# Kernel optimization log

Measured on AMD Instinct MI355X. Metric: run time of the kernel, lower is better.

The kernel has to match this reference:

```python
import jax, jax.numpy as jnp
import numpy as np

HID, KQ, V = 1024, 64, 64
B, S = 8, 2048
NEG_INF = -1000000000.0


def setup_inputs() -> dict:
    key = jax.random.key(0)
    ks = jax.random.split(key, 10)
    return {
        "k_hidden_inputs": jax.random.normal(ks[0], (B, S, HID), jnp.float32),
        "q_hidden_inputs": jax.random.normal(ks[1], (B, S, HID), jnp.float32),
        "v_hidden_inputs": jax.random.normal(ks[2], (B, S, HID), jnp.float32),
        "mask": jax.random.randint(ks[3], (B, S, S), 0, 2, jnp.int32),
        "Wq": jax.random.normal(ks[4], (HID, KQ), jnp.float32) * 0.02,
        "bq": jnp.zeros((KQ,), jnp.float32),
        "Wk": jax.random.normal(ks[5], (HID, KQ), jnp.float32) * 0.02,
        "bk": jnp.zeros((KQ,), jnp.float32),
        "Wv": jax.random.normal(ks[6], (HID, V), jnp.float32) * 0.02,
        "bv": jnp.zeros((V,), jnp.float32),
    }


def reference(k_hidden_inputs, q_hidden_inputs, v_hidden_inputs, mask,
              Wq, bq, Wk, bk, Wv, bv):
    keys = jnp.einsum('bsh,hd->bsd', k_hidden_inputs, Wk) + bk
    queries = jnp.einsum('bsh,hd->bsd', q_hidden_inputs, Wq) + bq
    values = jnp.einsum('bsh,hd->bsd', v_hidden_inputs, Wv) + bv
    # scaled dot-product scores: [B, S_q, S_k]
    scores = jnp.einsum('bqd,bkd->bqk', queries, keys) / jnp.sqrt(jnp.float32(KQ))
    scores = jnp.where(mask == 0, jnp.float32(NEG_INF), scores)
    attn = jax.nn.softmax(scores, axis=-1)
    return jnp.einsum('bqk,bkv->bqv', attn, values)
```

## Files before the change

### kernel.cpp

```cpp
#include <hip/hip_runtime.h>

#define HIDDEN 1024
#define NB 8
#define SEQ 2048
#define DH 64

typedef long long i64;
typedef unsigned short u16;
typedef __attribute__((ext_vector_type(8))) _Float16 half8;
typedef __attribute__((ext_vector_type(4))) float f32x4;

#define MFMA16F __builtin_amdgcn_mfma_f32_16x16x32_f16

__device__ __forceinline__ u16 f2h(float x) {
    _Float16 h = (_Float16)x;
    return __builtin_bit_cast(u16, h);
}
__device__ __forceinline__ void gl_lds16(const void* g, void* l) {
    __builtin_amdgcn_global_load_lds(
        (const __attribute__((address_space(1))) unsigned int*)g,
        (__attribute__((address_space(3))) unsigned int*)l, 16, 0, 0);
}

__global__ __launch_bounds__(256) void wimg_prep(
    const float* __restrict__ Wq, const float* __restrict__ Wk, const float* __restrict__ Wv,
    u16* __restrict__ Wimg)
{
    const int t = blockIdx.x * 256 + threadIdx.x;
    const int te = t >> 13;
    const int rem = t & 8191;
    const int n = rem >> 7;
    const int bb = rem & 127;
    const int kq = bb >> 5, bq = bb & 31;
    const float* W = te == 0 ? Wq : te == 1 ? Wk : Wv;
    const i64 base = ((i64)(te * 4 + kq) * 64 + n) * 256 + ((bq ^ (n & 7)) << 3);
    #pragma unroll
    for (int j = 0; j < 8; ++j) {
        const int k = kq * 256 + bq * 8 + j;
        Wimg[base + j] = f2h(W[(i64)k * DH + n]);
    }
}

__global__ __launch_bounds__(256) void proj_mfma7(
    const float* __restrict__ qh, const float* __restrict__ kh, const float* __restrict__ vh,
    const u16* __restrict__ Wimg,
    const float* __restrict__ bq, const float* __restrict__ bk, const float* __restrict__ bv,
    u16* __restrict__ Qb, u16* __restrict__ Kb, u16* __restrict__ Vt)
{
    const int te = blockIdx.y;
    const float* A    = te == 0 ? qh : te == 1 ? kh : vh;
    const float* bias = te == 0 ? bq : te == 1 ? bk : bv;
    const int row0 = blockIdx.x << 6;
    const int t = threadIdx.x;
    const int w = t >> 6, lane = t & 63;
    const int lr = lane & 15, lg = lane >> 4;

    __shared__ __attribute__((aligned(16))) u16 Wl[16384];

    const u16* Wte = Wimg + (i64)te * 4 * 16384;
    const float* arow = A + (i64)(row0 + w * 16 + lr) * HIDDEN + (lg << 3);

    f32x4 acc[4] = {};

    float4 buf0[2], buf1[2];
    buf0[0] = *(const float4*)(arow);
    buf0[1] = *(const float4*)(arow + 4);
    buf1[0] = *(const float4*)(arow + 32);
    buf1[1] = *(const float4*)(arow + 36);

#define CVT8(bf, a8) { \
        const float xs_[8] = {bf[0].x, bf[0].y, bf[0].z, bf[0].w, \
                              bf[1].x, bf[1].y, bf[1].z, bf[1].w}; \
        _Pragma("unroll") \
        for (int j_ = 0; j_ < 8; ++j_) a8[j_] = (_Float16)xs_[j_]; }

    #pragma unroll 1
    for (int kq = 0; kq < 4; ++kq) {
        if (kq) __syncthreads();
        {
            const u16* src = Wte + kq * 16384 + (w << 12) + (lane << 3);
            #pragma unroll
            for (int i = 0; i < 8; ++i)
                gl_lds16(src + i * 512, &Wl[(w << 12) + i * 512]);
        }
        asm volatile("s_waitcnt vmcnt(0)" ::: "memory");
        __syncthreads();

        #pragma unroll
        for (int s = 0; s < 8; ++s) {
            const int ks = kq * 8 + s;
            half8 a;
            if ((s & 1) == 0) {
                CVT8(buf0, a)
                const int kn = ((ks + 2) & 31) << 5;
                buf0[0] = *(const float4*)(arow + kn);
                buf0[1] = *(const float4*)(arow + kn + 4);
            } else {
                CVT8(buf1, a)
                const int kn = ((ks + 2) & 31) << 5;
                buf1[0] = *(const float4*)(arow + kn);
                buf1[1] = *(const float4*)(arow + kn + 4);
            }
            const int s4 = s << 2;
            #pragma unroll
            for (int nt = 0; nt < 4; ++nt) {
                const int n = nt * 16 + lr;
                const half8 b = *(const half8*)&Wl[n * 256 + (((s4 + lg) ^ (n & 7)) << 3)];
                acc[nt] = MFMA16F(a, b, acc[nt], 0, 0, 0);
            }
        }
    }
#undef CVT8

    #pragma unroll
    for (int nt = 0; nt < 4; ++nt) {
        const int col = nt * 16 + lr;
        const float bb = bias[col];
        #pragma unroll
        for (int r = 0; r < 4; ++r) {
            const i64 grow = row0 + w * 16 + (lg << 2) + r;
            const u16 v = f2h(acc[nt][r] + bb);
            if (te == 0)      Qb[grow * DH + col] = v;
            else if (te == 1) Kb[grow * DH + col] = v;
            else {
                const i64 bb2 = grow >> 11, key = grow & 2047;
                Vt[(bb2 * DH + col) * SEQ + key] = v;
            }
        }
    }
}

__global__ __launch_bounds__(64) void attn_mfma(
    const u16* __restrict__ Qb, const u16* __restrict__ Kb, const u16* __restrict__ Vt,
    const int* __restrict__ mask, float* __restrict__ out)
{
    __shared__ __attribute__((aligned(16))) u16 Kl[2][64 * 64];
    __shared__ __attribute__((aligned(16))) u16 Vl[2][64 * 64];
    __shared__ __attribute__((aligned(16))) u16 Pl[16][72];

    const int lane = threadIdx.x;
    const int lr = lane & 15, lg = lane >> 4;
    const int b  = blockIdx.x >> 7;
    const int q0 = (blockIdx.x & 127) << 4;

    const i64 qrow = (i64)b * SEQ + q0 + lr;
    const half8 qf0 = *(const half8*)(Qb + qrow * DH + lg * 8);
    const half8 qf1 = *(const half8*)(Qb + qrow * DH + 32 + lg * 8);

    const int srow = lane >> 3;
    const int scb  = lane & 7;

    f32x4 oacc[4] = {};
    float rs0 = 0.f, rs1 = 0.f, rs2 = 0.f, rs3 = 0.f;

    {
        const i64 kbase = (i64)b * SEQ;
        #pragma unroll
        for (int i = 0; i < 8; ++i) {
            int row = i * 8 + srow, cb = scb ^ (row & 7);
            gl_lds16(Kb + (kbase + row) * DH + cb * 8, &Kl[0][i * 512]);
        }
        #pragma unroll
        for (int i = 0; i < 8; ++i) {
            int row = i * 8 + srow, cb = scb ^ (row & 7);
            gl_lds16(Vt + ((i64)b * DH + row) * SEQ + cb * 8, &Vl[0][i * 512]);
        }
    }

    #pragma unroll 1
    for (int t = 0; t < 32; ++t) {
        const int kt = t * 64;
        const int buf = t & 1;

        int mv[16];
        #pragma unroll
        for (int tt = 0; tt < 4; ++tt)
            #pragma unroll
            for (int r = 0; r < 4; ++r)
                mv[tt * 4 + r] =
                    mask[((i64)b * SEQ + q0 + lg * 4 + r) * SEQ + kt + tt * 16 + lr];

        if (t < 31) {
            const int kn = kt + 64;
            const i64 kbase = (i64)b * SEQ + kn;
            #pragma unroll
            for (int i = 0; i < 8; ++i) {
                int row = i * 8 + srow, cb = scb ^ (row & 7);
                gl_lds16(Kb + (kbase + row) * DH + cb * 8, &Kl[buf ^ 1][i * 512]);
            }
            #pragma unroll
            for (int i = 0; i < 8; ++i) {
                int row = i * 8 + srow, cb = scb ^ (row & 7);
                gl_lds16(Vt + ((i64)b * DH + row) * SEQ + kn + cb * 8, &Vl[buf ^ 1][i * 512]);
            }
            asm volatile("s_waitcnt vmcnt(32)" ::: "memory");
        } else {
            asm volatile("s_waitcnt vmcnt(16)" ::: "memory");
        }

        f32x4 sacc[4] = {};
        #pragma unroll
        for (int tt = 0; tt < 4; ++tt) {
            int row = tt * 16 + lr, x = row & 7;
            half8 k0 = *(const half8*)&Kl[buf][row * 64 + ((lg) ^ x) * 8];
            half8 k1 = *(const half8*)&Kl[buf][row * 64 + ((lg + 4) ^ x) * 8];
            sacc[tt] = MFMA16F(qf0, k0, sacc[tt], 0, 0, 0);
            sacc[tt] = MFMA16F(qf1, k1, sacc[tt], 0, 0, 0);
        }

        #pragma unroll
        for (int tt = 0; tt < 4; ++tt) {
            #pragma unroll
            for (int r = 0; r < 4; ++r) {
                float p = (mv[tt * 4 + r] != 0) ? __expf(sacc[tt][r] * 0.125f) : 0.0f;
                if      (r == 0) rs0 += p;
                else if (r == 1) rs1 += p;
                else if (r == 2) rs2 += p;
                else             rs3 += p;
                Pl[lg * 4 + r][tt * 16 + lr] = f2h(p);
            }
        }

        const half8 p0 = *(const half8*)&Pl[lr][lg * 8];
        const half8 p1 = *(const half8*)&Pl[lr][32 + lg * 8];
        #pragma unroll
        for (int vt = 0; vt < 4; ++vt) {
            int row = vt * 16 + lr, x = row & 7;
            half8 v0 = *(const half8*)&Vl[buf][row * 64 + ((lg) ^ x) * 8];
            half8 v1 = *(const half8*)&Vl[buf][row * 64 + ((lg + 4) ^ x) * 8];
            oacc[vt] = MFMA16F(p0, v0, oacc[vt], 0, 0, 0);
            oacc[vt] = MFMA16F(p1, v1, oacc[vt], 0, 0, 0);
        }
    }

    float rs[4] = {rs0, rs1, rs2, rs3};
    #pragma unroll
    for (int r = 0; r < 4; ++r) {
        float v = rs[r];
        v += __shfl_xor(v, 1, 64);
        v += __shfl_xor(v, 2, 64);
        v += __shfl_xor(v, 4, 64);
        v += __shfl_xor(v, 8, 64);
        rs[r] = 1.0f / v;
    }
    #pragma unroll
    for (int vt = 0; vt < 4; ++vt)
        #pragma unroll
        for (int r = 0; r < 4; ++r)
            out[((i64)b * SEQ + q0 + lg * 4 + r) * DH + vt * 16 + lr] = oacc[vt][r] * rs[r];
}

extern "C" void kernel_launch(void* const* d_in, const int* in_sizes, int n_in,
                              void* d_out, int out_size, void* d_ws, size_t ws_size,
                              hipStream_t stream) {
    const float* kh   = (const float*)d_in[0];
    const float* qh   = (const float*)d_in[1];
    const float* vh   = (const float*)d_in[2];
    const int*   mask = (const int*)  d_in[3];
    const float* Wq   = (const float*)d_in[4];
    const float* bq   = (const float*)d_in[5];
    const float* Wk   = (const float*)d_in[6];
    const float* bk   = (const float*)d_in[7];
    const float* Wv   = (const float*)d_in[8];
    const float* bv   = (const float*)d_in[9];
    float* out = (float*)d_out;

    u16* Wimg = (u16*)d_ws;
    u16* Qb   = Wimg + 3 * 4 * 16384;
    u16* Kb   = Qb + (i64)NB * SEQ * DH;
    u16* Vt   = Kb + (i64)NB * SEQ * DH;

    wimg_prep<<<96, 256, 0, stream>>>(Wq, Wk, Wv, Wimg);
    proj_mfma7<<<dim3(256, 3), 256, 0, stream>>>(qh, kh, vh, Wimg,
                                                 bq, bk, bv, Qb, Kb, Vt);
    attn_mfma<<<1024, 64, 0, stream>>>(Qb, Kb, Vt, mask, out);
}
```

Baseline: 120.9 us.

## Restructure projection GEMM with double-buffered LDS staging of activations and weights

The projection kernel now stages both the fp32 activation tile and the fp16 weight tile into LDS with async global-to-LDS loads, double-buffered over 8 K-chunks of 128. Previously only the weights went through LDS and activations were register-prefetched from global. Blocks are halved to 32 rows, each wave owning a 16x32 output sub-tile, which doubles the grid to 1536 blocks. The weight image layout is reorganised into 128-wide K chunks to match. This aims to overlap memory loads with MFMA work and raise occupancy, at the cost of more LDS use per block and reading each weight chunk twice as often.

```diff
diff --git a/kernel.cpp b/kernel.cpp
--- a/kernel.cpp
+++ b/kernel.cpp
@@ -22,26 +22,27 @@
         (__attribute__((address_space(3))) unsigned int*)l, 16, 0, 0);
 }
 
-__global__ __launch_bounds__(256) void wimg_prep(
+__global__ __launch_bounds__(256) void wimg_prep8(
     const float* __restrict__ Wq, const float* __restrict__ Wk, const float* __restrict__ Wv,
     u16* __restrict__ Wimg)
 {
     const int t = blockIdx.x * 256 + threadIdx.x;
     const int te = t >> 13;
     const int rem = t & 8191;
-    const int n = rem >> 7;
-    const int bb = rem & 127;
-    const int kq = bb >> 5, bq = bb & 31;
+    const int p = rem >> 10;
+    const int rem2 = rem & 1023;
+    const int n = rem2 >> 4;
+    const int pos = rem2 & 15;
     const float* W = te == 0 ? Wq : te == 1 ? Wk : Wv;
-    const i64 base = ((i64)(te * 4 + kq) * 64 + n) * 256 + ((bq ^ (n & 7)) << 3);
-    #pragma unroll
-    for (int j = 0; j < 8; ++j) {
-        const int k = kq * 256 + bq * 8 + j;
-        Wimg[base + j] = f2h(W[(i64)k * DH + n]);
-    }
-}
-
-__global__ __launch_bounds__(256) void proj_mfma7(
+    const int g = pos ^ (n & 7);
+    const int k0 = p * 128 + g * 8;
+    u16* dst = Wimg + (i64)t * 8;
+    #pragma unroll
+    for (int j = 0; j < 8; ++j)
+        dst[j] = f2h(W[(i64)(k0 + j) * DH + n]);
+}
+
+__global__ __launch_bounds__(256) void proj_mfma8(
     const float* __restrict__ qh, const float* __restrict__ kh, const float* __restrict__ vh,
     const u16* __restrict__ Wimg,
     const float* __restrict__ bq, const float* __restrict__ bk, const float* __restrict__ bv,
@@ -50,75 +51,82 @@
     const int te = blockIdx.y;
     const float* A    = te == 0 ? qh : te == 1 ? kh : vh;
     const float* bias = te == 0 ? bq : te == 1 ? bk : bv;
-    const int row0 = blockIdx.x << 6;
+    const int row0 = blockIdx.x << 5;
     const int t = threadIdx.x;
     const int w = t >> 6, lane = t & 63;
     const int lr = lane & 15, lg = lane >> 4;
-
-    __shared__ __attribute__((aligned(16))) u16 Wl[16384];
-
-    const u16* Wte = Wimg + (i64)te * 4 * 16384;
-    const float* arow = A + (i64)(row0 + w * 16 + lr) * HIDDEN + (lg << 3);
-
-    f32x4 acc[4] = {};
-
-    float4 buf0[2], buf1[2];
-    buf0[0] = *(const float4*)(arow);
-    buf0[1] = *(const float4*)(arow + 4);
-    buf1[0] = *(const float4*)(arow + 32);
-    buf1[1] = *(const float4*)(arow + 36);
-
-#define CVT8(bf, a8) { \
-        const float xs_[8] = {bf[0].x, bf[0].y, bf[0].z, bf[0].w, \
-                              bf[1].x, bf[1].y, bf[1].z, bf[1].w}; \
+    const int wr = (w & 1) << 4;
+    const int wc = (w >> 1) << 5;
+
+    __shared__ __attribute__((aligned(16))) float AL[2][32 * 128];
+    __shared__ __attribute__((aligned(16))) u16  WL[2][64 * 128];
+
+    const u16* Wte = Wimg + (i64)te * 8 * 8192;
+
+    const float* asrc[4]; int adst[4];
+    #pragma unroll
+    for (int i = 0; i < 4; ++i) {
+        const int r0 = 8 * w + 2 * i;
+        const int rl = r0 + (lane >> 5);
+        asrc[i] = A + (i64)(row0 + rl) * HIDDEN + (((lane & 31) ^ (rl & 7)) << 2);
+        adst[i] = r0 * 128;
+    }
+    const u16* wsrc[4]; int wdst[4];
+    #pragma unroll
+    for (int i = 0; i < 4; ++i) {
+        const int n0 = 16 * w + 4 * i;
+        wsrc[i] = Wte + n0 * 128 + (lane << 3);
+        wdst[i] = n0 * 128;
+    }
+
+    f32x4 acc[2] = {};
+
+#define STAGE8(bufi, p) { \
         _Pragma("unroll") \
-        for (int j_ = 0; j_ < 8; ++j_) a8[j_] = (_Float16)xs_[j_]; }
-
+        for (int i_ = 0; i_ < 4; ++i_) \
+            gl_lds16(asrc[i_] + (p) * 128, &AL[bufi][adst[i_]]); \
+        _Pragma("unroll") \
+        for (int i_ = 0; i_ < 4; ++i_) \
+            gl_lds16(wsrc[i_] + (p) * 8192, &WL[bufi][wdst[i_]]); }
+
+    STAGE8(0, 0)
+
+    int buf = 0;
     #pragma unroll 1
-    for (int kq = 0; kq < 4; ++kq) {
-        if (kq) __syncthreads();
-        {
-            const u16* src = Wte + kq * 16384 + (w << 12) + (lane << 3);
-            #pragma unroll
-            for (int i = 0; i < 8; ++i)
-                gl_lds16(src + i * 512, &Wl[(w << 12) + i * 512]);
-        }
+    for (int p = 0; p < 8; ++p) {
         asm volatile("s_waitcnt vmcnt(0)" ::: "memory");
         __syncthreads();
-
-        #pragma unroll
-        for (int s = 0; s < 8; ++s) {
-            const int ks = kq * 8 + s;
+        if (p < 7) STAGE8(buf ^ 1, p + 1)
+        const int x = lr & 7;
+        #pragma unroll
+        for (int ks = 0; ks < 4; ++ks) {
+            const int b0 = ks * 8 + lg * 2;
+            const float4 fa = *(const float4*)&AL[buf][(wr + lr) * 128 + ((b0 ^ x) << 2)];
+            const float4 fb = *(const float4*)&AL[buf][(wr + lr) * 128 + (((b0 + 1) ^ x) << 2)];
             half8 a;
-            if ((s & 1) == 0) {
-                CVT8(buf0, a)
-                const int kn = ((ks + 2) & 31) << 5;
-                buf0[0] = *(const float4*)(arow + kn);
-                buf0[1] = *(const float4*)(arow + kn + 4);
-            } else {
-                CVT8(buf1, a)
-                const int kn = ((ks + 2) & 31) << 5;
-                buf1[0] = *(const float4*)(arow + kn);
-                buf1[1] = *(const float4*)(arow + kn + 4);
-            }
-            const int s4 = s << 2;
-            #pragma unroll
-            for (int nt = 0; nt < 4; ++nt) {
-                const int n = nt * 16 + lr;
-                const half8 b = *(const half8*)&Wl[n * 256 + (((s4 + lg) ^ (n & 7)) << 3)];
-                acc[nt] = MFMA16F(a, b, acc[nt], 0, 0, 0);
-            }
-        }
-    }
-#undef CVT8
-
-    #pragma unroll
-    for (int nt = 0; nt < 4; ++nt) {
-        const int col = nt * 16 + lr;
+            a[0] = (_Float16)fa.x; a[1] = (_Float16)fa.y;
+            a[2] = (_Float16)fa.z; a[3] = (_Float16)fa.w;
+            a[4] = (_Float16)fb.x; a[5] = (_Float16)fb.y;
+            a[6] = (_Float16)fb.z; a[7] = (_Float16)fb.w;
+            #pragma unroll
+            for (int nt = 0; nt < 2; ++nt) {
+                const int n = wc + nt * 16 + lr;
+                const int pos = (ks * 4 + lg) ^ x;
+                const half8 bfr = *(const half8*)&WL[buf][n * 128 + (pos << 3)];
+                acc[nt] = MFMA16F(a, bfr, acc[nt], 0, 0, 0);
+            }
+        }
+        buf ^= 1;
+    }
+#undef STAGE8
+
+    #pragma unroll
+    for (int nt = 0; nt < 2; ++nt) {
+        const int col = wc + nt * 16 + lr;
         const float bb = bias[col];
         #pragma unroll
         for (int r = 0; r < 4; ++r) {
-            const i64 grow = row0 + w * 16 + (lg << 2) + r;
+            const i64 grow = row0 + wr + (lg << 2) + r;
             const u16 v = f2h(acc[nt][r] + bb);
             if (te == 0)      Qb[grow * DH + col] = v;
             else if (te == 1) Kb[grow * DH + col] = v;
@@ -266,12 +274,12 @@
     float* out = (float*)d_out;
 
     u16* Wimg = (u16*)d_ws;
-    u16* Qb   = Wimg + 3 * 4 * 16384;
+    u16* Qb   = Wimg + 3 * 8 * 8192;
     u16* Kb   = Qb + (i64)NB * SEQ * DH;
     u16* Vt   = Kb + (i64)NB * SEQ * DH;
 
-    wimg_prep<<<96, 256, 0, stream>>>(Wq, Wk, Wv, Wimg);
-    proj_mfma7<<<dim3(256, 3), 256, 0, stream>>>(qh, kh, vh, Wimg,
+    wimg_prep8<<<96, 256, 0, stream>>>(Wq, Wk, Wv, Wimg);
+    proj_mfma8<<<dim3(512, 3), 256, 0, stream>>>(qh, kh, vh, Wimg,
                                                  bq, bk, bv, Qb, Kb, Vt);
     attn_mfma<<<1024, 64, 0, stream>>>(Qb, Kb, Vt, mask, out);
 }
```

Result: faster. 115.0 us (-4.9%).

## Double-buffer weight chunks in LDS with smaller projection blocks

Applied to the files above, without the earlier changes.

The projection kernel now works on 32 rows per block with 128 threads, and it walks K in 16 chunks of 64. Weight chunks are staged into two alternating LDS buffers, and the next chunk's activations are prefetched while the current chunk is computed. The weight image is re-laid out into 64-wide K chunks with an XOR swizzle to match. The goal is to overlap global weight staging with MFMA work, shrink LDS use from 32KB to 16KB per block, and raise the number of blocks in flight. In exchange there are more barriers per row tile, and weight traffic per row doubles. The code also has no explicit vmcnt wait before the barrier, so it depends on in-order completion of the vector memory loads.

```diff
diff --git a/kernel.cpp b/kernel.cpp
--- a/kernel.cpp
+++ b/kernel.cpp
@@ -22,26 +22,27 @@
         (__attribute__((address_space(3))) unsigned int*)l, 16, 0, 0);
 }
 
-__global__ __launch_bounds__(256) void wimg_prep(
+__global__ __launch_bounds__(256) void wimg_prep16(
     const float* __restrict__ Wq, const float* __restrict__ Wk, const float* __restrict__ Wv,
     u16* __restrict__ Wimg)
 {
     const int t = blockIdx.x * 256 + threadIdx.x;
     const int te = t >> 13;
     const int rem = t & 8191;
-    const int n = rem >> 7;
-    const int bb = rem & 127;
-    const int kq = bb >> 5, bq = bb & 31;
+    const int p = rem >> 9;
+    const int rem2 = rem & 511;
+    const int n = rem2 >> 3;
+    const int pos = rem2 & 7;
     const float* W = te == 0 ? Wq : te == 1 ? Wk : Wv;
-    const i64 base = ((i64)(te * 4 + kq) * 64 + n) * 256 + ((bq ^ (n & 7)) << 3);
-    #pragma unroll
-    for (int j = 0; j < 8; ++j) {
-        const int k = kq * 256 + bq * 8 + j;
-        Wimg[base + j] = f2h(W[(i64)k * DH + n]);
-    }
-}
-
-__global__ __launch_bounds__(256) void proj_mfma7(
+    const int g = pos ^ (n & 7);
+    const int k0 = p * 64 + g * 8;
+    u16* dst = Wimg + (i64)t * 8;
+    #pragma unroll
+    for (int j = 0; j < 8; ++j)
+        dst[j] = f2h(W[(i64)(k0 + j) * DH + n]);
+}
+
+__global__ __launch_bounds__(128) void proj_mfma9(
     const float* __restrict__ qh, const float* __restrict__ kh, const float* __restrict__ vh,
     const u16* __restrict__ Wimg,
     const float* __restrict__ bq, const float* __restrict__ bk, const float* __restrict__ bv,
@@ -50,67 +51,81 @@
     const int te = blockIdx.y;
     const float* A    = te == 0 ? qh : te == 1 ? kh : vh;
     const float* bias = te == 0 ? bq : te == 1 ? bk : bv;
-    const int row0 = blockIdx.x << 6;
+    const int row0 = blockIdx.x << 5;
     const int t = threadIdx.x;
     const int w = t >> 6, lane = t & 63;
     const int lr = lane & 15, lg = lane >> 4;
 
-    __shared__ __attribute__((aligned(16))) u16 Wl[16384];
-
-    const u16* Wte = Wimg + (i64)te * 4 * 16384;
+    __shared__ __attribute__((aligned(16))) u16 WL[2][4096];
+
+    const u16* Wte = Wimg + (i64)te * 16 * 4096;
     const float* arow = A + (i64)(row0 + w * 16 + lr) * HIDDEN + (lg << 3);
 
     f32x4 acc[4] = {};
 
-    float4 buf0[2], buf1[2];
-    buf0[0] = *(const float4*)(arow);
-    buf0[1] = *(const float4*)(arow + 4);
-    buf1[0] = *(const float4*)(arow + 32);
-    buf1[1] = *(const float4*)(arow + 36);
-
-#define CVT8(bf, a8) { \
-        const float xs_[8] = {bf[0].x, bf[0].y, bf[0].z, bf[0].w, \
-                              bf[1].x, bf[1].y, bf[1].z, bf[1].w}; \
-        _Pragma("unroll") \
-        for (int j_ = 0; j_ < 8; ++j_) a8[j_] = (_Float16)xs_[j_]; }
+#define STAGEW(P, B) { \
+        _Pragma("unroll") \
+        for (int i_ = 0; i_ < 4; ++i_) { \
+            const int off_ = ((w << 2) + i_) << 9; \
+            gl_lds16(Wte + ((P) << 12) + off_ + (lane << 3), &WL[B][off_ + (lane << 3) - (lane << 3)] + off_ * 0 + 0); \
+        } }
+#undef STAGEW
+#define STAGEW(P, B) { \
+        _Pragma("unroll") \
+        for (int i_ = 0; i_ < 4; ++i_) { \
+            const int off_ = ((w << 2) + i_) << 9; \
+            gl_lds16(Wte + ((P) << 12) + off_ + (lane << 3), &WL[B][off_]); \
+        } }
+
+#define LOADA(P, r00, r01, r10, r11) { \
+        const int kb_ = ((P) & 15) << 6; \
+        r00 = *(const float4*)(arow + kb_); \
+        r01 = *(const float4*)(arow + kb_ + 4); \
+        r10 = *(const float4*)(arow + kb_ + 32); \
+        r11 = *(const float4*)(arow + kb_ + 36); }
+
+#define COMPUTE(B, r00, r01, r10, r11) { \
+        half8 a0_, a1_; \
+        a0_[0] = (_Float16)r00.x; a0_[1] = (_Float16)r00.y; \
+        a0_[2] = (_Float16)r00.z; a0_[3] = (_Float16)r00.w; \
+        a0_[4] = (_Float16)r01.x; a0_[5] = (_Float16)r01.y; \
+        a0_[6] = (_Float16)r01.z; a0_[7] = (_Float16)r01.w; \
+        a1_[0] = (_Float16)r10.x; a1_[1] = (_Float16)r10.y; \
+        a1_[2] = (_Float16)r10.z; a1_[3] = (_Float16)r10.w; \
+        a1_[4] = (_Float16)r11.x; a1_[5] = (_Float16)r11.y; \
+        a1_[6] = (_Float16)r11.z; a1_[7] = (_Float16)r11.w; \
+        _Pragma("unroll") \
+        for (int nt_ = 0; nt_ < 4; ++nt_) { \
+            const int n_ = nt_ * 16 + lr; \
+            const half8 b0_ = *(const half8*)&WL[B][n_ * 64 + (((lg) ^ (n_ & 7)) << 3)]; \
+            acc[nt_] = MFMA16F(a0_, b0_, acc[nt_], 0, 0, 0); \
+        } \
+        _Pragma("unroll") \
+        for (int nt_ = 0; nt_ < 4; ++nt_) { \
+            const int n_ = nt_ * 16 + lr; \
+            const half8 b1_ = *(const half8*)&WL[B][n_ * 64 + ((((4 + lg)) ^ (n_ & 7)) << 3)]; \
+            acc[nt_] = MFMA16F(a1_, b1_, acc[nt_], 0, 0, 0); \
+        } }
+
+    float4 e00, e01, e10, e11, o00, o01, o10, o11;
+
+    STAGEW(0, 0)
+    LOADA(0, e00, e01, e10, e11)
 
     #pragma unroll 1
-    for (int kq = 0; kq < 4; ++kq) {
-        if (kq) __syncthreads();
-        {
-            const u16* src = Wte + kq * 16384 + (w << 12) + (lane << 3);
-            #pragma unroll
-            for (int i = 0; i < 8; ++i)
-                gl_lds16(src + i * 512, &Wl[(w << 12) + i * 512]);
-        }
-        asm volatile("s_waitcnt vmcnt(0)" ::: "memory");
+    for (int p2 = 0; p2 < 16; p2 += 2) {
         __syncthreads();
-
-        #pragma unroll
-        for (int s = 0; s < 8; ++s) {
-            const int ks = kq * 8 + s;
-            half8 a;
-            if ((s & 1) == 0) {
-                CVT8(buf0, a)
-                const int kn = ((ks + 2) & 31) << 5;
-                buf0[0] = *(const float4*)(arow + kn);
-                buf0[1] = *(const float4*)(arow + kn + 4);
-            } else {
-                CVT8(buf1, a)
-                const int kn = ((ks + 2) & 31) << 5;
-                buf1[0] = *(const float4*)(arow + kn);
-                buf1[1] = *(const float4*)(arow + kn + 4);
-            }
-            const int s4 = s << 2;
-            #pragma unroll
-            for (int nt = 0; nt < 4; ++nt) {
-                const int n = nt * 16 + lr;
-                const half8 b = *(const half8*)&Wl[n * 256 + (((s4 + lg) ^ (n & 7)) << 3)];
-                acc[nt] = MFMA16F(a, b, acc[nt], 0, 0, 0);
-            }
-        }
-    }
-#undef CVT8
+        STAGEW((p2 + 1) & 15, 1)
+        LOADA(p2 + 1, o00, o01, o10, o11)
+        COMPUTE(0, e00, e01, e10, e11)
+        __syncthreads();
+        STAGEW((p2 + 2) & 15, 0)
+        LOADA(p2 + 2, e00, e01, e10, e11)
+        COMPUTE(1, o00, o01, o10, o11)
+    }
+#undef STAGEW
+#undef LOADA
+#undef COMPUTE
 
     #pragma unroll
     for (int nt = 0; nt < 4; ++nt) {
@@ -266,12 +281,12 @@
     float* out = (float*)d_out;
 
     u16* Wimg = (u16*)d_ws;
-    u16* Qb   = Wimg + 3 * 4 * 16384;
+    u16* Qb   = Wimg + 3 * 16 * 4096;
     u16* Kb   = Qb + (i64)NB * SEQ * DH;
     u16* Vt   = Kb + (i64)NB * SEQ * DH;
 
-    wimg_prep<<<96, 256, 0, stream>>>(Wq, Wk, Wv, Wimg);
-    proj_mfma7<<<dim3(256, 3), 256, 0, stream>>>(qh, kh, vh, Wimg,
+    wimg_prep16<<<96, 256, 0, stream>>>(Wq, Wk, Wv, Wimg);
+    proj_mfma9<<<dim3(512, 3), 128, 0, stream>>>(qh, kh, vh, Wimg,
                                                  bq, bk, bv, Qb, Kb, Vt);
     attn_mfma<<<1024, 64, 0, stream>>>(Qb, Kb, Vt, mask, out);
 }
```

Result: no change. 122.4 us (+1.2%).
